# Performance work log

Hardware: AMD Instinct MI355X
Metric: run time of the kernel (lower is better)

Reference implementation:

```python
import jax, jax.numpy as jnp
import numpy as np

B, S, DM = 2, 2048, 1024
H, DH = 16, 64
SCALE = jnp.sqrt(jnp.float32(DH))  # dot_scale = sqrt(dim_head)


def setup_inputs() -> dict:
    key = jax.random.key(0)
    ks = jax.random.split(key, 9)
    std = 1.0 / np.sqrt(DM)
    x = jax.random.normal(ks[0], (B, S, DM), dtype=jnp.float32)
    Wq = jax.random.uniform(ks[1], (DM, DM), jnp.float32, -std, std)
    bq = jax.random.uniform(ks[2], (DM,), jnp.float32, -std, std)
    Wk = jax.random.uniform(ks[3], (DM, DM), jnp.float32, -std, std)
    bk = jax.random.uniform(ks[4], (DM,), jnp.float32, -std, std)
    Wv = jax.random.uniform(ks[5], (DM, DM), jnp.float32, -std, std)
    bv = jax.random.uniform(ks[6], (DM,), jnp.float32, -std, std)
    Wo = jax.random.uniform(ks[7], (DM, DM), jnp.float32, -std, std)
    bo = jax.random.uniform(ks[8], (DM,), jnp.float32, -std, std)
    # causal mask: 1 = masked (future positions), broadcast over batch
    causal = jnp.triu(jnp.ones((S, S), dtype=jnp.int32), k=1)
    attention_mask = jnp.broadcast_to(causal, (B, S, S))
    return {"x": x, "Wq": Wq, "bq": bq, "Wk": Wk, "bk": bk,
            "Wv": Wv, "bv": bv, "Wo": Wo, "bo": bo,
            "attention_mask": attention_mask}


def reference(x, Wq, bq, Wk, bk, Wv, bv, Wo, bo, attention_mask):
    # Linear layers (torch nn.Linear: y = x @ W^T + b)
    q = (x @ Wq.T + bq).reshape(B, S, H, DH).transpose(0, 2, 1, 3)  # (B,H,S,DH)
    k = (x @ Wk.T + bk).reshape(B, S, H, DH).transpose(0, 2, 1, 3)  # (B,H,S,DH)
    v = (x @ Wv.T + bv).reshape(B, S, H, DH).transpose(0, 2, 1, 3)  # (B,H,S,DH)
    # scores: (B,H,S,S), then mask==1 -> -inf, softmax over last dim
    scores = jnp.einsum('bhsd,bhtd->bhst', q, k) / SCALE
    mask = attention_mask[:, None, :, :]  # (B,1,S,S)
    scores = jnp.where(mask == 1, -jnp.inf, scores)
    attn = jax.nn.softmax(scores, axis=-1)
    # dropout is identity in eval mode
    ctx = jnp.einsum('bhst,bhtd->bshd', attn, v).reshape(B, S, H * DH)
    return ctx @ Wo.T + bo
```

## Files before the change

kernel.cpp:

```cpp
#include <hip/hip_runtime.h>
#include <stdint.h>

typedef unsigned short u16;
typedef __attribute__((ext_vector_type(8))) short bf16x8;
typedef __attribute__((ext_vector_type(4))) float f32x4;

#define BATCH 2
#define S_LEN 2048
#define DMODEL 1024
#define NH 16
#define DHEAD 64
#define MTOT 4096
#define QSCALE 0.18033688011112042f
#define PSTR 132

#define GL2LDS(g, l) \
  __builtin_amdgcn_global_load_lds((const __attribute__((address_space(1))) void*)(g), \
                                   (__attribute__((address_space(3))) void*)(l), 16, 0, 0)

__device__ __forceinline__ u16 f2bf(float x) {
  union { float f; uint32_t u; } v; v.f = x;
  uint32_t r = v.u + 0x7fffu + ((v.u >> 16) & 1u);
  return (u16)(r >> 16);
}
__device__ __forceinline__ u16 f2bf_fast(float x) {
  union { float f; uint32_t u; } v; v.f = x;
  return (u16)((v.u + 0x8000u) >> 16);
}

struct CvtArgs {
  const float* src[5];
  u16* dst[5];
};

__global__ __launch_bounds__(256) void cvt_all(CvtArgs a) {
  int bx = blockIdx.x;
  int region, off;
  if (bx < 4096) { region = 0; off = bx; }
  else { region = 1 + ((bx - 4096) >> 10); off = (bx - 4096) & 1023; }
  const float* s = a.src[region];
  u16* d = a.dst[region];
  int i = (off * 256 + threadIdx.x) * 4;
  float4 v = *(const float4*)(s + i);
  uint2 pk;
  pk.x = (uint32_t)f2bf(v.x) | ((uint32_t)f2bf(v.y) << 16);
  pk.y = (uint32_t)f2bf(v.z) | ((uint32_t)f2bf(v.w) << 16);
  *(uint2*)(d + i) = pk;
}

__device__ __forceinline__ void gemm_body(const u16* __restrict__ A,
                                          const u16* __restrict__ W,
                                          const float* __restrict__ bias,
                                          void* __restrict__ out,
                                          int mode, float scale) {
  __shared__ u16 As[128 * 32];
  __shared__ u16 Bs[128 * 32];
  const int tid = threadIdx.x;
  const int m0 = blockIdx.y * 128;
  const int n0 = blockIdx.x * 128;
  const int wave = tid >> 6, lane = tid & 63;
  const int wm = (wave >> 1) * 64, wn = (wave & 1) * 64;
  const int quad = lane >> 4, l15 = lane & 15;

  const int row0 = tid >> 2, k80 = (tid & 3) * 8;
  const int row1 = (tid + 256) >> 2;
  const int lb0 = wave * 512;
  const int lb1 = 2048 + wave * 512;

  f32x4 acc[4][4] = {};

  for (int kt = 0; kt < DMODEL; kt += 32) {
    GL2LDS(A + (size_t)(m0 + row0) * DMODEL + kt + k80, As + lb0);
    GL2LDS(A + (size_t)(m0 + row1) * DMODEL + kt + k80, As + lb1);
    GL2LDS(W + (size_t)(n0 + row0) * DMODEL + kt + k80, Bs + lb0);
    GL2LDS(W + (size_t)(n0 + row1) * DMODEL + kt + k80, Bs + lb1);
    __syncthreads();
    bf16x8 af[4], bfr[4];
#pragma unroll
    for (int bi = 0; bi < 4; ++bi)
      af[bi] = *(const bf16x8*)(&As[(wm + bi * 16 + l15) * 32 + quad * 8]);
#pragma unroll
    for (int bj = 0; bj < 4; ++bj)
      bfr[bj] = *(const bf16x8*)(&Bs[(wn + bj * 16 + l15) * 32 + quad * 8]);
#pragma unroll
    for (int bi = 0; bi < 4; ++bi)
#pragma unroll
      for (int bj = 0; bj < 4; ++bj)
        acc[bi][bj] = __builtin_amdgcn_mfma_f32_16x16x32_bf16(af[bi], bfr[bj], acc[bi][bj], 0, 0, 0);
    __syncthreads();
  }

#pragma unroll
  for (int bi = 0; bi < 4; ++bi) {
#pragma unroll
    for (int bj = 0; bj < 4; ++bj) {
      int n = n0 + wn + bj * 16 + l15;
      float bval = bias[n];
#pragma unroll
      for (int r = 0; r < 4; ++r) {
        int m = m0 + wm + bi * 16 + quad * 4 + r;
        float v = (acc[bi][bj][r] + bval) * scale;
        u16 bvu = f2bf(v);
        int b = m >> 11, s = m & 2047;
        int h = n >> 6, d = n & 63;
        size_t bh = (size_t)(b * NH + h);
        if (mode == 1)
          ((u16*)out)[(bh * S_LEN + s) * DHEAD + d] = bvu;
        else
          ((u16*)out)[((bh * 256 + (s >> 3)) * 64 + d) * 8 + (s & 7)] = bvu;
      }
    }
  }
}

struct QKVArgs {
  const u16* w[3];
  const float* b[3];
  u16* o[3];
};

__global__ __launch_bounds__(256) void qkv_gemm(const u16* __restrict__ xb, QKVArgs a) {
  int z = blockIdx.z;
  int mode = (z == 2) ? 2 : 1;
  float scale = (z == 0) ? QSCALE : 1.0f;
  gemm_body(xb, a.w[z], a.b[z], a.o[z], mode, scale);
}

__global__ __launch_bounds__(256) void out_gemm(const u16* __restrict__ A,
                                                const u16* __restrict__ W,
                                                const float* __restrict__ bias,
                                                float* __restrict__ out) {
  __shared__ u16 As[128 * 32];
  __shared__ u16 Bs[64 * 32];
  const int tid = threadIdx.x;
  const int m0 = blockIdx.y * 128;
  const int n0 = blockIdx.x * 64;
  const int wave = tid >> 6, lane = tid & 63;
  const int wm = (wave >> 1) * 64, wn = (wave & 1) * 32;
  const int quad = lane >> 4, l15 = lane & 15;

  const int row0 = tid >> 2, k80 = (tid & 3) * 8;
  const int row1 = (tid + 256) >> 2;
  const int lb0 = wave * 512;
  const int lb1 = 2048 + wave * 512;

  f32x4 acc[4][2] = {};

  for (int kt = 0; kt < DMODEL; kt += 32) {
    GL2LDS(A + (size_t)(m0 + row0) * DMODEL + kt + k80, As + lb0);
    GL2LDS(A + (size_t)(m0 + row1) * DMODEL + kt + k80, As + lb1);
    GL2LDS(W + (size_t)(n0 + row0) * DMODEL + kt + k80, Bs + lb0);
    __syncthreads();
    bf16x8 af[4], bfr[2];
#pragma unroll
    for (int bi = 0; bi < 4; ++bi)
      af[bi] = *(const bf16x8*)(&As[(wm + bi * 16 + l15) * 32 + quad * 8]);
#pragma unroll
    for (int bj = 0; bj < 2; ++bj)
      bfr[bj] = *(const bf16x8*)(&Bs[(wn + bj * 16 + l15) * 32 + quad * 8]);
#pragma unroll
    for (int bi = 0; bi < 4; ++bi)
#pragma unroll
      for (int bj = 0; bj < 2; ++bj)
        acc[bi][bj] = __builtin_amdgcn_mfma_f32_16x16x32_bf16(af[bi], bfr[bj], acc[bi][bj], 0, 0, 0);
    __syncthreads();
  }

#pragma unroll
  for (int bi = 0; bi < 4; ++bi) {
#pragma unroll
    for (int bj = 0; bj < 2; ++bj) {
      int n = n0 + wn + bj * 16 + l15;
      float bval = bias[n];
#pragma unroll
      for (int r = 0; r < 4; ++r) {
        int m = m0 + wm + bi * 16 + quad * 4 + r;
        out[(size_t)m * DMODEL + n] = acc[bi][bj][r] + bval;
      }
    }
  }
}

__global__ __launch_bounds__(256) void attn(const u16* __restrict__ Q,
                                            const u16* __restrict__ Kg,
                                            const u16* __restrict__ Vt8,
                                            u16* __restrict__ ctx) {
  __shared__ u16 Ks[128 * 72];
  __shared__ u16 Vs[64 * 136];
  __shared__ u16 Ps[64 * PSTR];
  const int tid = threadIdx.x;
  const int qp = blockIdx.x >> 5;
  const int bh = blockIdx.x & 31;
  const int wave = tid >> 6, lane = tid & 63;
  const int quad = lane >> 4, l15 = lane & 15;
  const size_t base = (size_t)bh * S_LEN * DHEAD;
  const int b = bh >> 4, h = bh & 15;

  for (int half = 0; half < 2; ++half) {
    const int qt = half ? (S_LEN / 64 - 1 - qp) : qp;
    const int qrow = qt * 64 + wave * 16 + l15;
    bf16x8 qf0 = *(const bf16x8*)(Q + base + (size_t)qrow * DHEAD + quad * 8);
    bf16x8 qf1 = *(const bf16x8*)(Q + base + (size_t)qrow * DHEAD + 32 + quad * 8);

    float l_part[4] = {0.f, 0.f, 0.f, 0.f};
    f32x4 o[4] = {};

    const int ktmax = qt >> 1;
    for (int kt = 0; kt <= ktmax; ++kt) {
#pragma unroll
      for (int i = 0; i < 4; ++i) {
        int cc = tid + 256 * i;
        {
          int row = cc >> 3, k8 = (cc & 7) * 8;
          uint4 v = *(const uint4*)(Kg + base + (size_t)(kt * 128 + row) * DHEAD + k8);
          *(uint4*)(&Ks[row * 72 + k8]) = v;
        }
        {
          int d = cc & 63, oc = cc >> 6;
          uint4 v = *(const uint4*)(Vt8 + base + (((size_t)(kt * 16 + oc)) * 64 + d) * 8);
          *(uint4*)(&Vs[d * 136 + oc * 8]) = v;
        }
      }
      __syncthreads();

      const bool diag = (kt == ktmax);
      const int qg_max = qt * 64 + wave * 16 + 15;
      f32x4 s_acc[8];
#pragma unroll
      for (int bj = 0; bj < 8; ++bj) {
        if (diag && (kt * 128 + bj * 16 > qg_max)) {
          s_acc[bj] = f32x4{-1e30f, -1e30f, -1e30f, -1e30f};
          continue;
        }
        bf16x8 kf0 = *(const bf16x8*)(&Ks[(bj * 16 + l15) * 72 + quad * 8]);
        bf16x8 kf1 = *(const bf16x8*)(&Ks[(bj * 16 + l15) * 72 + 32 + quad * 8]);
        f32x4 t = {0.f, 0.f, 0.f, 0.f};
        t = __builtin_amdgcn_mfma_f32_16x16x32_bf16(qf0, kf0, t, 0, 0, 0);
        t = __builtin_amdgcn_mfma_f32_16x16x32_bf16(qf1, kf1, t, 0, 0, 0);
        s_acc[bj] = t;
      }

      if (diag) {
#pragma unroll
        for (int bj = 0; bj < 8; ++bj) {
          int kg = kt * 128 + bj * 16 + l15;
#pragma unroll
          for (int r = 0; r < 4; ++r) {
            int qg = qt * 64 + wave * 16 + quad * 4 + r;
            if (kg > qg) s_acc[bj][r] = -1e30f;
          }
        }
      }

#pragma unroll
      for (int bj = 0; bj < 8; ++bj) {
#pragma unroll
        for (int r = 0; r < 4; ++r) {
          float p = exp2f(s_acc[bj][r]);
          l_part[r] += p;
          Ps[(wave * 16 + quad * 4 + r) * PSTR + bj * 16 + l15] = f2bf_fast(p);
        }
      }

#pragma unroll
      for (int kk = 0; kk < 4; ++kk) {
        bf16x8 pf = *(const bf16x8*)(&Ps[(wave * 16 + l15) * PSTR + kk * 32 + quad * 8]);
#pragma unroll
        for (int dj = 0; dj < 4; ++dj) {
          bf16x8 vf = *(const bf16x8*)(&Vs[(dj * 16 + l15) * 136 + kk * 32 + quad * 8]);
          o[dj] = __builtin_amdgcn_mfma_f32_16x16x32_bf16(pf, vf, o[dj], 0, 0, 0);
        }
      }
      __syncthreads();
    }

#pragma unroll
    for (int r = 0; r < 4; ++r) {
      float s = l_part[r];
      s += __shfl_xor(s, 1, 64);
      s += __shfl_xor(s, 2, 64);
      s += __shfl_xor(s, 4, 64);
      s += __shfl_xor(s, 8, 64);
      float inv = 1.0f / s;
      int srow = qt * 64 + wave * 16 + quad * 4 + r;
      size_t rowbase = ((size_t)b * S_LEN + srow) * DMODEL + h * DHEAD;
#pragma unroll
      for (int dj = 0; dj < 4; ++dj)
        ctx[rowbase + dj * 16 + l15] = f2bf(o[dj][r] * inv);
    }
  }
}

extern "C" void kernel_launch(void* const* d_in, const int* in_sizes, int n_in,
                              void* d_out, int out_size, void* d_ws, size_t ws_size,
                              hipStream_t stream) {
  const float* x  = (const float*)d_in[0];
  const float* Wq = (const float*)d_in[1];
  const float* bq = (const float*)d_in[2];
  const float* Wk = (const float*)d_in[3];
  const float* bk = (const float*)d_in[4];
  const float* Wv = (const float*)d_in[5];
  const float* bv = (const float*)d_in[6];
  const float* Wo = (const float*)d_in[7];
  const float* bo = (const float*)d_in[8];
  float* out = (float*)d_out;

  char* ws = (char*)d_ws;
  const size_t MB = 1u << 20;
  u16* xb   = (u16*)(ws + 0);
  u16* ctxb = xb;
  u16* wqb  = (u16*)(ws + 8 * MB);
  u16* wkb  = (u16*)(ws + 10 * MB);
  u16* wvb  = (u16*)(ws + 12 * MB);
  u16* wob  = (u16*)(ws + 14 * MB);
  u16* qb   = (u16*)(ws + 16 * MB);
  u16* kb   = (u16*)(ws + 24 * MB);
  u16* vtb  = (u16*)(ws + 32 * MB);

  CvtArgs c;
  c.src[0] = x;  c.dst[0] = xb;
  c.src[1] = Wq; c.dst[1] = wqb;
  c.src[2] = Wk; c.dst[2] = wkb;
  c.src[3] = Wv; c.dst[3] = wvb;
  c.src[4] = Wo; c.dst[4] = wob;
  cvt_all<<<4096 + 4 * 1024, 256, 0, stream>>>(c);

  QKVArgs a;
  a.w[0] = wqb; a.w[1] = wkb; a.w[2] = wvb;
  a.b[0] = bq;  a.b[1] = bk;  a.b[2] = bv;
  a.o[0] = qb;  a.o[1] = kb;  a.o[2] = vtb;
  qkv_gemm<<<dim3(DMODEL / 128, MTOT / 128, 3), 256, 0, stream>>>(xb, a);

  attn<<<512, 256, 0, stream>>>(qb, kb, vtb, ctxb);

  out_gemm<<<dim3(DMODEL / 64, MTOT / 128), 256, 0, stream>>>(ctxb, wob, bo, out);
}
```

Before: 224.2 us.

## Double GEMM K-tile with XOR-swizzled LDS; split attention to one q-tile per block

Both GEMMs now load 64-wide K tiles per barrier pair, using an XOR swizzle on the LDS column chunk to avoid bank conflicts. This halves the number of sync points per K sweep. The attention kernel drops its paired front/back q-tile loop and launches one block per q-tile, heaviest tiles first. It also aliases the P scratch buffer onto the K tile (with an added barrier) to cut LDS use and raise occupancy. The trade-off is an extra __syncthreads per KV step and a less even per-block workload in attention.

```diff
diff --git a/kernel.cpp b/kernel.cpp
--- a/kernel.cpp
+++ b/kernel.cpp
@@ -53,8 +53,8 @@
                                           const float* __restrict__ bias,
                                           void* __restrict__ out,
                                           int mode, float scale) {
-  __shared__ u16 As[128 * 32];
-  __shared__ u16 Bs[128 * 32];
+  __shared__ u16 As[128 * 64];
+  __shared__ u16 Bs[128 * 64];
   const int tid = threadIdx.x;
   const int m0 = blockIdx.y * 128;
   const int n0 = blockIdx.x * 128;
@@ -62,31 +62,34 @@
   const int wm = (wave >> 1) * 64, wn = (wave & 1) * 64;
   const int quad = lane >> 4, l15 = lane & 15;
 
-  const int row0 = tid >> 2, k80 = (tid & 3) * 8;
-  const int row1 = (tid + 256) >> 2;
-  const int lb0 = wave * 512;
-  const int lb1 = 2048 + wave * 512;
+  const int rr = tid >> 3;
+  const int cl = ((tid & 7) ^ (rr & 7)) * 8;
+  const int xr = (l15 & 7);
 
   f32x4 acc[4][4] = {};
 
-  for (int kt = 0; kt < DMODEL; kt += 32) {
-    GL2LDS(A + (size_t)(m0 + row0) * DMODEL + kt + k80, As + lb0);
-    GL2LDS(A + (size_t)(m0 + row1) * DMODEL + kt + k80, As + lb1);
-    GL2LDS(W + (size_t)(n0 + row0) * DMODEL + kt + k80, Bs + lb0);
-    GL2LDS(W + (size_t)(n0 + row1) * DMODEL + kt + k80, Bs + lb1);
-    __syncthreads();
-    bf16x8 af[4], bfr[4];
-#pragma unroll
-    for (int bi = 0; bi < 4; ++bi)
-      af[bi] = *(const bf16x8*)(&As[(wm + bi * 16 + l15) * 32 + quad * 8]);
-#pragma unroll
-    for (int bj = 0; bj < 4; ++bj)
-      bfr[bj] = *(const bf16x8*)(&Bs[(wn + bj * 16 + l15) * 32 + quad * 8]);
-#pragma unroll
-    for (int bi = 0; bi < 4; ++bi)
+  for (int kt = 0; kt < DMODEL; kt += 64) {
+#pragma unroll
+    for (int j = 0; j < 4; ++j) {
+      GL2LDS(A + (size_t)(m0 + j * 32 + rr) * DMODEL + kt + cl, As + j * 2048 + wave * 512);
+      GL2LDS(W + (size_t)(n0 + j * 32 + rr) * DMODEL + kt + cl, Bs + j * 2048 + wave * 512);
+    }
+    __syncthreads();
+#pragma unroll
+    for (int h = 0; h < 2; ++h) {
+      bf16x8 af[4], bfr[4];
+#pragma unroll
+      for (int bi = 0; bi < 4; ++bi)
+        af[bi] = *(const bf16x8*)(&As[(wm + bi * 16 + l15) * 64 + (((h * 4 + quad) ^ xr) * 8)]);
 #pragma unroll
       for (int bj = 0; bj < 4; ++bj)
-        acc[bi][bj] = __builtin_amdgcn_mfma_f32_16x16x32_bf16(af[bi], bfr[bj], acc[bi][bj], 0, 0, 0);
+        bfr[bj] = *(const bf16x8*)(&Bs[(wn + bj * 16 + l15) * 64 + (((h * 4 + quad) ^ xr) * 8)]);
+#pragma unroll
+      for (int bi = 0; bi < 4; ++bi)
+#pragma unroll
+        for (int bj = 0; bj < 4; ++bj)
+          acc[bi][bj] = __builtin_amdgcn_mfma_f32_16x16x32_bf16(af[bi], bfr[bj], acc[bi][bj], 0, 0, 0);
+    }
     __syncthreads();
   }
 
@@ -130,8 +133,8 @@
                                                 const u16* __restrict__ W,
                                                 const float* __restrict__ bias,
                                                 float* __restrict__ out) {
-  __shared__ u16 As[128 * 32];
-  __shared__ u16 Bs[64 * 32];
+  __shared__ u16 As[128 * 64];
+  __shared__ u16 Bs[64 * 64];
   const int tid = threadIdx.x;
   const int m0 = blockIdx.y * 128;
   const int n0 = blockIdx.x * 64;
@@ -139,30 +142,35 @@
   const int wm = (wave >> 1) * 64, wn = (wave & 1) * 32;
   const int quad = lane >> 4, l15 = lane & 15;
 
-  const int row0 = tid >> 2, k80 = (tid & 3) * 8;
-  const int row1 = (tid + 256) >> 2;
-  const int lb0 = wave * 512;
-  const int lb1 = 2048 + wave * 512;
+  const int rr = tid >> 3;
+  const int cl = ((tid & 7) ^ (rr & 7)) * 8;
+  const int xr = (l15 & 7);
 
   f32x4 acc[4][2] = {};
 
-  for (int kt = 0; kt < DMODEL; kt += 32) {
-    GL2LDS(A + (size_t)(m0 + row0) * DMODEL + kt + k80, As + lb0);
-    GL2LDS(A + (size_t)(m0 + row1) * DMODEL + kt + k80, As + lb1);
-    GL2LDS(W + (size_t)(n0 + row0) * DMODEL + kt + k80, Bs + lb0);
-    __syncthreads();
-    bf16x8 af[4], bfr[2];
-#pragma unroll
-    for (int bi = 0; bi < 4; ++bi)
-      af[bi] = *(const bf16x8*)(&As[(wm + bi * 16 + l15) * 32 + quad * 8]);
-#pragma unroll
-    for (int bj = 0; bj < 2; ++bj)
-      bfr[bj] = *(const bf16x8*)(&Bs[(wn + bj * 16 + l15) * 32 + quad * 8]);
-#pragma unroll
-    for (int bi = 0; bi < 4; ++bi)
+  for (int kt = 0; kt < DMODEL; kt += 64) {
+#pragma unroll
+    for (int j = 0; j < 4; ++j)
+      GL2LDS(A + (size_t)(m0 + j * 32 + rr) * DMODEL + kt + cl, As + j * 2048 + wave * 512);
+#pragma unroll
+    for (int j = 0; j < 2; ++j)
+      GL2LDS(W + (size_t)(n0 + j * 32 + rr) * DMODEL + kt + cl, Bs + j * 2048 + wave * 512);
+    __syncthreads();
+#pragma unroll
+    for (int h = 0; h < 2; ++h) {
+      bf16x8 af[4], bfr[2];
+#pragma unroll
+      for (int bi = 0; bi < 4; ++bi)
+        af[bi] = *(const bf16x8*)(&As[(wm + bi * 16 + l15) * 64 + (((h * 4 + quad) ^ xr) * 8)]);
 #pragma unroll
       for (int bj = 0; bj < 2; ++bj)
-        acc[bi][bj] = __builtin_amdgcn_mfma_f32_16x16x32_bf16(af[bi], bfr[bj], acc[bi][bj], 0, 0, 0);
+        bfr[bj] = *(const bf16x8*)(&Bs[(wn + bj * 16 + l15) * 64 + (((h * 4 + quad) ^ xr) * 8)]);
+#pragma unroll
+      for (int bi = 0; bi < 4; ++bi)
+#pragma unroll
+        for (int bj = 0; bj < 2; ++bj)
+          acc[bi][bj] = __builtin_amdgcn_mfma_f32_16x16x32_bf16(af[bi], bfr[bj], acc[bi][bj], 0, 0, 0);
+    }
     __syncthreads();
   }
 
@@ -187,73 +195,78 @@
                                             u16* __restrict__ ctx) {
   __shared__ u16 Ks[128 * 72];
   __shared__ u16 Vs[64 * 136];
-  __shared__ u16 Ps[64 * PSTR];
+  u16* Ps = Ks;
   const int tid = threadIdx.x;
-  const int qp = blockIdx.x >> 5;
+  const int qt = 31 - (blockIdx.x >> 5);
   const int bh = blockIdx.x & 31;
   const int wave = tid >> 6, lane = tid & 63;
   const int quad = lane >> 4, l15 = lane & 15;
   const size_t base = (size_t)bh * S_LEN * DHEAD;
   const int b = bh >> 4, h = bh & 15;
 
-  for (int half = 0; half < 2; ++half) {
-    const int qt = half ? (S_LEN / 64 - 1 - qp) : qp;
-    const int qrow = qt * 64 + wave * 16 + l15;
-    bf16x8 qf0 = *(const bf16x8*)(Q + base + (size_t)qrow * DHEAD + quad * 8);
-    bf16x8 qf1 = *(const bf16x8*)(Q + base + (size_t)qrow * DHEAD + 32 + quad * 8);
-
-    float l_part[4] = {0.f, 0.f, 0.f, 0.f};
-    f32x4 o[4] = {};
-
-    const int ktmax = qt >> 1;
-    for (int kt = 0; kt <= ktmax; ++kt) {
-#pragma unroll
-      for (int i = 0; i < 4; ++i) {
-        int cc = tid + 256 * i;
-        {
-          int row = cc >> 3, k8 = (cc & 7) * 8;
-          uint4 v = *(const uint4*)(Kg + base + (size_t)(kt * 128 + row) * DHEAD + k8);
-          *(uint4*)(&Ks[row * 72 + k8]) = v;
+  const int qrow = qt * 64 + wave * 16 + l15;
+  bf16x8 qf0 = *(const bf16x8*)(Q + base + (size_t)qrow * DHEAD + quad * 8);
+  bf16x8 qf1 = *(const bf16x8*)(Q + base + (size_t)qrow * DHEAD + 32 + quad * 8);
+
+  float l_part[4] = {0.f, 0.f, 0.f, 0.f};
+  f32x4 o[4] = {};
+
+  const int ktmax = qt >> 1;
+  for (int kt = 0; kt <= ktmax; ++kt) {
+#pragma unroll
+    for (int i = 0; i < 4; ++i) {
+      int cc = tid + 256 * i;
+      {
+        int row = cc >> 3, k8 = (cc & 7) * 8;
+        uint4 v = *(const uint4*)(Kg + base + (size_t)(kt * 128 + row) * DHEAD + k8);
+        *(uint4*)(&Ks[row * 72 + k8]) = v;
+      }
+      {
+        int d = cc & 63, oc = cc >> 6;
+        uint4 v = *(const uint4*)(Vt8 + base + (((size_t)(kt * 16 + oc)) * 64 + d) * 8);
+        *(uint4*)(&Vs[d * 136 + oc * 8]) = v;
+      }
+    }
+    __syncthreads();
+
+    const bool diag = (kt == ktmax);
+    const int qg_max = qt * 64 + wave * 16 + 15;
+    f32x4 s_acc[8];
+#pragma unroll
+    for (int bj = 0; bj < 8; ++bj) {
+      if (diag && (kt * 128 + bj * 16 > qg_max)) {
+        s_acc[bj] = f32x4{-1e30f, -1e30f, -1e30f, -1e30f};
+        continue;
+      }
+      bf16x8 kf0 = *(const bf16x8*)(&Ks[(bj * 16 + l15) * 72 + quad * 8]);
+      bf16x8 kf1 = *(const bf16x8*)(&Ks[(bj * 16 + l15) * 72 + 32 + quad * 8]);
+      f32x4 t = {0.f, 0.f, 0.f, 0.f};
+      t = __builtin_amdgcn_mfma_f32_16x16x32_bf16(qf0, kf0, t, 0, 0, 0);
+      t = __builtin_amdgcn_mfma_f32_16x16x32_bf16(qf1, kf1, t, 0, 0, 0);
+      s_acc[bj] = t;
+    }
+
+    if (diag) {
+#pragma unroll
+      for (int bj = 0; bj < 8; ++bj) {
+        int kg = kt * 128 + bj * 16 + l15;
+#pragma unroll
+        for (int r = 0; r < 4; ++r) {
+          int qg = qt * 64 + wave * 16 + quad * 4 + r;
+          if (kg > qg) s_acc[bj][r] = -1e30f;
         }
-        {
-          int d = cc & 63, oc = cc >> 6;
-          uint4 v = *(const uint4*)(Vt8 + base + (((size_t)(kt * 16 + oc)) * 64 + d) * 8);
-          *(uint4*)(&Vs[d * 136 + oc * 8]) = v;
-        }
-      }
-      __syncthreads();
-
-      const bool diag = (kt == ktmax);
-      const int qg_max = qt * 64 + wave * 16 + 15;
-      f32x4 s_acc[8];
-#pragma unroll
-      for (int bj = 0; bj < 8; ++bj) {
-        if (diag && (kt * 128 + bj * 16 > qg_max)) {
-          s_acc[bj] = f32x4{-1e30f, -1e30f, -1e30f, -1e30f};
-          continue;
-        }
-        bf16x8 kf0 = *(const bf16x8*)(&Ks[(bj * 16 + l15) * 72 + quad * 8]);
-        bf16x8 kf1 = *(const bf16x8*)(&Ks[(bj * 16 + l15) * 72 + 32 + quad * 8]);
-        f32x4 t = {0.f, 0.f, 0.f, 0.f};
-        t = __builtin_amdgcn_mfma_f32_16x16x32_bf16(qf0, kf0, t, 0, 0, 0);
-        t = __builtin_amdgcn_mfma_f32_16x16x32_bf16(qf1, kf1, t, 0, 0, 0);
-        s_acc[bj] = t;
-      }
-
-      if (diag) {
-#pragma unroll
-        for (int bj = 0; bj < 8; ++bj) {
-          int kg = kt * 128 + bj * 16 + l15;
-#pragma unroll
-          for (int r = 0; r < 4; ++r) {
-            int qg = qt * 64 + wave * 16 + quad * 4 + r;
-            if (kg > qg) s_acc[bj][r] = -1e30f;
-          }
-        }
-      }
-
-#pragma unroll
-      for (int bj = 0; bj < 8; ++bj) {
+      }
+    }
+
+    __syncthreads();
+
+#pragma unroll
+    for (int bj = 0; bj < 8; ++bj) {
+      if (diag && (kt * 128 + bj * 16 > qg_max)) {
+#pragma unroll
+        for (int r = 0; r < 4; ++r)
+          Ps[(wave * 16 + quad * 4 + r) * PSTR + bj * 16 + l15] = 0;
+      } else {
 #pragma unroll
         for (int r = 0; r < 4; ++r) {
           float p = exp2f(s_acc[bj][r]);
@@ -261,33 +274,33 @@
           Ps[(wave * 16 + quad * 4 + r) * PSTR + bj * 16 + l15] = f2bf_fast(p);
         }
       }
-
-#pragma unroll
-      for (int kk = 0; kk < 4; ++kk) {
-        bf16x8 pf = *(const bf16x8*)(&Ps[(wave * 16 + l15) * PSTR + kk * 32 + quad * 8]);
-#pragma unroll
-        for (int dj = 0; dj < 4; ++dj) {
-          bf16x8 vf = *(const bf16x8*)(&Vs[(dj * 16 + l15) * 136 + kk * 32 + quad * 8]);
-          o[dj] = __builtin_amdgcn_mfma_f32_16x16x32_bf16(pf, vf, o[dj], 0, 0, 0);
-        }
-      }
-      __syncthreads();
-    }
-
-#pragma unroll
-    for (int r = 0; r < 4; ++r) {
-      float s = l_part[r];
-      s += __shfl_xor(s, 1, 64);
-      s += __shfl_xor(s, 2, 64);
-      s += __shfl_xor(s, 4, 64);
-      s += __shfl_xor(s, 8, 64);
-      float inv = 1.0f / s;
-      int srow = qt * 64 + wave * 16 + quad * 4 + r;
-      size_t rowbase = ((size_t)b * S_LEN + srow) * DMODEL + h * DHEAD;
-#pragma unroll
-      for (int dj = 0; dj < 4; ++dj)
-        ctx[rowbase + dj * 16 + l15] = f2bf(o[dj][r] * inv);
-    }
+    }
+
+#pragma unroll
+    for (int kk = 0; kk < 4; ++kk) {
+      bf16x8 pf = *(const bf16x8*)(&Ps[(wave * 16 + l15) * PSTR + kk * 32 + quad * 8]);
+#pragma unroll
+      for (int dj = 0; dj < 4; ++dj) {
+        bf16x8 vf = *(const bf16x8*)(&Vs[(dj * 16 + l15) * 136 + kk * 32 + quad * 8]);
+        o[dj] = __builtin_amdgcn_mfma_f32_16x16x32_bf16(pf, vf, o[dj], 0, 0, 0);
+      }
+    }
+    __syncthreads();
+  }
+
+#pragma unroll
+  for (int r = 0; r < 4; ++r) {
+    float s = l_part[r];
+    s += __shfl_xor(s, 1, 64);
+    s += __shfl_xor(s, 2, 64);
+    s += __shfl_xor(s, 4, 64);
+    s += __shfl_xor(s, 8, 64);
+    float inv = 1.0f / s;
+    int srow = qt * 64 + wave * 16 + quad * 4 + r;
+    size_t rowbase = ((size_t)b * S_LEN + srow) * DMODEL + h * DHEAD;
+#pragma unroll
+    for (int dj = 0; dj < 4; ++dj)
+      ctx[rowbase + dj * 16 + l15] = f2bf(o[dj][r] * inv);
   }
 }
 
@@ -331,7 +344,7 @@
   a.o[0] = qb;  a.o[1] = kb;  a.o[2] = vtb;
   qkv_gemm<<<dim3(DMODEL / 128, MTOT / 128, 3), 256, 0, stream>>>(xb, a);
 
-  attn<<<512, 256, 0, stream>>>(qb, kb, vtb, ctxb);
+  attn<<<1024, 256, 0, stream>>>(qb, kb, vtb, ctxb);
 
   out_gemm<<<dim3(DMODEL / 64, MTOT / 128), 256, 0, stream>>>(ctxb, wob, bo, out);
 }
```

After: 243.7 us. 8.7% more time.

## Double-buffer attention K/V via direct-to-LDS loads and XOR-swizzle GEMM LDS tiles

Applied to the files above, without the earlier changes.

The attention kernel now stages K and V tiles with global_load_lds into double-buffered LDS, prefetching the next tile while the current one is computed. It drops the per-tile trailing barrier. K rows use an XOR swizzle to avoid bank conflicts, and V is read in its native 8-packed layout. The PV step is split into two 64-key halves so fully masked halves on the diagonal tile skip their exp and MFMA work. Both GEMMs also XOR-swizzle their LDS tile columns to reduce bank conflicts on fragment reads. The cost is more LDS use, which may lower occupancy, plus the sync correctness of the single-barrier pipeline and the reuse of the P buffer.

```diff
diff --git a/kernel.cpp b/kernel.cpp
--- a/kernel.cpp
+++ b/kernel.cpp
@@ -12,7 +12,6 @@
 #define DHEAD 64
 #define MTOT 4096
 #define QSCALE 0.18033688011112042f
-#define PSTR 132
 
 #define GL2LDS(g, l) \
   __builtin_amdgcn_global_load_lds((const __attribute__((address_space(1))) void*)(g), \
@@ -62,26 +61,27 @@
   const int wm = (wave >> 1) * 64, wn = (wave & 1) * 64;
   const int quad = lane >> 4, l15 = lane & 15;
 
-  const int row0 = tid >> 2, k80 = (tid & 3) * 8;
-  const int row1 = (tid + 256) >> 2;
+  const int row0 = tid >> 2, g0 = ((tid & 3) ^ (row0 & 3)) * 8;
+  const int row1 = (tid + 256) >> 2, g1 = ((tid & 3) ^ (row1 & 3)) * 8;
   const int lb0 = wave * 512;
   const int lb1 = 2048 + wave * 512;
+  const int xk = (quad ^ (l15 & 3)) * 8;
 
   f32x4 acc[4][4] = {};
 
   for (int kt = 0; kt < DMODEL; kt += 32) {
-    GL2LDS(A + (size_t)(m0 + row0) * DMODEL + kt + k80, As + lb0);
-    GL2LDS(A + (size_t)(m0 + row1) * DMODEL + kt + k80, As + lb1);
-    GL2LDS(W + (size_t)(n0 + row0) * DMODEL + kt + k80, Bs + lb0);
-    GL2LDS(W + (size_t)(n0 + row1) * DMODEL + kt + k80, Bs + lb1);
+    GL2LDS(A + (size_t)(m0 + row0) * DMODEL + kt + g0, As + lb0);
+    GL2LDS(A + (size_t)(m0 + row1) * DMODEL + kt + g1, As + lb1);
+    GL2LDS(W + (size_t)(n0 + row0) * DMODEL + kt + g0, Bs + lb0);
+    GL2LDS(W + (size_t)(n0 + row1) * DMODEL + kt + g1, Bs + lb1);
     __syncthreads();
     bf16x8 af[4], bfr[4];
 #pragma unroll
     for (int bi = 0; bi < 4; ++bi)
-      af[bi] = *(const bf16x8*)(&As[(wm + bi * 16 + l15) * 32 + quad * 8]);
+      af[bi] = *(const bf16x8*)(&As[(wm + bi * 16 + l15) * 32 + xk]);
 #pragma unroll
     for (int bj = 0; bj < 4; ++bj)
-      bfr[bj] = *(const bf16x8*)(&Bs[(wn + bj * 16 + l15) * 32 + quad * 8]);
+      bfr[bj] = *(const bf16x8*)(&Bs[(wn + bj * 16 + l15) * 32 + xk]);
 #pragma unroll
     for (int bi = 0; bi < 4; ++bi)
 #pragma unroll
@@ -139,25 +139,26 @@
   const int wm = (wave >> 1) * 64, wn = (wave & 1) * 32;
   const int quad = lane >> 4, l15 = lane & 15;
 
-  const int row0 = tid >> 2, k80 = (tid & 3) * 8;
-  const int row1 = (tid + 256) >> 2;
+  const int row0 = tid >> 2, g0 = ((tid & 3) ^ (row0 & 3)) * 8;
+  const int row1 = (tid + 256) >> 2, g1 = ((tid & 3) ^ (row1 & 3)) * 8;
   const int lb0 = wave * 512;
   const int lb1 = 2048 + wave * 512;
+  const int xk = (quad ^ (l15 & 3)) * 8;
 
   f32x4 acc[4][2] = {};
 
   for (int kt = 0; kt < DMODEL; kt += 32) {
-    GL2LDS(A + (size_t)(m0 + row0) * DMODEL + kt + k80, As + lb0);
-    GL2LDS(A + (size_t)(m0 + row1) * DMODEL + kt + k80, As + lb1);
-    GL2LDS(W + (size_t)(n0 + row0) * DMODEL + kt + k80, Bs + lb0);
+    GL2LDS(A + (size_t)(m0 + row0) * DMODEL + kt + g0, As + lb0);
+    GL2LDS(A + (size_t)(m0 + row1) * DMODEL + kt + g1, As + lb1);
+    GL2LDS(W + (size_t)(n0 + row0) * DMODEL + kt + g0, Bs + lb0);
     __syncthreads();
     bf16x8 af[4], bfr[2];
 #pragma unroll
     for (int bi = 0; bi < 4; ++bi)
-      af[bi] = *(const bf16x8*)(&As[(wm + bi * 16 + l15) * 32 + quad * 8]);
+      af[bi] = *(const bf16x8*)(&As[(wm + bi * 16 + l15) * 32 + xk]);
 #pragma unroll
     for (int bj = 0; bj < 2; ++bj)
-      bfr[bj] = *(const bf16x8*)(&Bs[(wn + bj * 16 + l15) * 32 + quad * 8]);
+      bfr[bj] = *(const bf16x8*)(&Bs[(wn + bj * 16 + l15) * 32 + xk]);
 #pragma unroll
     for (int bi = 0; bi < 4; ++bi)
 #pragma unroll
@@ -185,9 +186,9 @@
                                             const u16* __restrict__ Kg,
                                             const u16* __restrict__ Vt8,
                                             u16* __restrict__ ctx) {
-  __shared__ u16 Ks[128 * 72];
-  __shared__ u16 Vs[64 * 136];
-  __shared__ u16 Ps[64 * PSTR];
+  __shared__ u16 Kd[2][128 * 64];
+  __shared__ u16 Vd[2][64 * 128];
+  __shared__ u16 Ps[64 * 80];
   const int tid = threadIdx.x;
   const int qp = blockIdx.x >> 5;
   const int bh = blockIdx.x & 31;
@@ -195,9 +196,23 @@
   const int quad = lane >> 4, l15 = lane & 15;
   const size_t base = (size_t)bh * S_LEN * DHEAD;
   const int b = bh >> 4, h = bh & 15;
+  const int xk7 = l15 & 7;
+
+#define STAGE(kt_, pb)                                                                   \
+  do {                                                                                   \
+    _Pragma("unroll")                                                                    \
+    for (int i_ = 0; i_ < 4; ++i_) {                                                     \
+      int c_ = tid + 256 * i_;                                                           \
+      int row_ = c_ >> 3, g_ = ((c_ & 7) ^ (row_ & 7)) * 8;                              \
+      GL2LDS(Kg + base + (size_t)((kt_) * 128 + row_) * 64 + g_,                         \
+             &Kd[pb][0] + i_ * 2048 + wave * 512);                                       \
+      GL2LDS(Vt8 + base + (size_t)((kt_) * 1024 + c_) * 8,                               \
+             &Vd[pb][0] + i_ * 2048 + wave * 512);                                       \
+    }                                                                                    \
+  } while (0)
 
   for (int half = 0; half < 2; ++half) {
-    const int qt = half ? (S_LEN / 64 - 1 - qp) : qp;
+    const int qt = half ? (31 - qp) : qp;
     const int qrow = qt * 64 + wave * 16 + l15;
     bf16x8 qf0 = *(const bf16x8*)(Q + base + (size_t)qrow * DHEAD + quad * 8);
     bf16x8 qf1 = *(const bf16x8*)(Q + base + (size_t)qrow * DHEAD + 32 + quad * 8);
@@ -206,22 +221,12 @@
     f32x4 o[4] = {};
 
     const int ktmax = qt >> 1;
+    STAGE(0, 0);
+
     for (int kt = 0; kt <= ktmax; ++kt) {
-#pragma unroll
-      for (int i = 0; i < 4; ++i) {
-        int cc = tid + 256 * i;
-        {
-          int row = cc >> 3, k8 = (cc & 7) * 8;
-          uint4 v = *(const uint4*)(Kg + base + (size_t)(kt * 128 + row) * DHEAD + k8);
-          *(uint4*)(&Ks[row * 72 + k8]) = v;
-        }
-        {
-          int d = cc & 63, oc = cc >> 6;
-          uint4 v = *(const uint4*)(Vt8 + base + (((size_t)(kt * 16 + oc)) * 64 + d) * 8);
-          *(uint4*)(&Vs[d * 136 + oc * 8]) = v;
-        }
-      }
+      const int p = kt & 1;
       __syncthreads();
+      if (kt < ktmax) STAGE(kt + 1, p ^ 1);
 
       const bool diag = (kt == ktmax);
       const int qg_max = qt * 64 + wave * 16 + 15;
@@ -232,8 +237,9 @@
           s_acc[bj] = f32x4{-1e30f, -1e30f, -1e30f, -1e30f};
           continue;
         }
-        bf16x8 kf0 = *(const bf16x8*)(&Ks[(bj * 16 + l15) * 72 + quad * 8]);
-        bf16x8 kf1 = *(const bf16x8*)(&Ks[(bj * 16 + l15) * 72 + 32 + quad * 8]);
+        const int krow = (bj * 16 + l15) * 64;
+        bf16x8 kf0 = *(const bf16x8*)(&Kd[p][krow + ((quad ^ xk7) * 8)]);
+        bf16x8 kf1 = *(const bf16x8*)(&Kd[p][krow + (((quad + 4) ^ xk7) * 8)]);
         f32x4 t = {0.f, 0.f, 0.f, 0.f};
         t = __builtin_amdgcn_mfma_f32_16x16x32_bf16(qf0, kf0, t, 0, 0, 0);
         t = __builtin_amdgcn_mfma_f32_16x16x32_bf16(qf1, kf1, t, 0, 0, 0);
@@ -253,26 +259,32 @@
       }
 
 #pragma unroll
-      for (int bj = 0; bj < 8; ++bj) {
-#pragma unroll
-        for (int r = 0; r < 4; ++r) {
-          float p = exp2f(s_acc[bj][r]);
-          l_part[r] += p;
-          Ps[(wave * 16 + quad * 4 + r) * PSTR + bj * 16 + l15] = f2bf_fast(p);
+      for (int ph = 0; ph < 2; ++ph) {
+        if (diag && (kt * 128 + ph * 64 > qg_max)) continue;
+#pragma unroll
+        for (int bj2 = 0; bj2 < 4; ++bj2) {
+          int bj = ph * 4 + bj2;
+#pragma unroll
+          for (int r = 0; r < 4; ++r) {
+            float pv = exp2f(s_acc[bj][r]);
+            l_part[r] += pv;
+            Ps[(wave * 16 + quad * 4 + r) * 80 + bj2 * 16 + l15] = f2bf_fast(pv);
+          }
         }
-      }
-
-#pragma unroll
-      for (int kk = 0; kk < 4; ++kk) {
-        bf16x8 pf = *(const bf16x8*)(&Ps[(wave * 16 + l15) * PSTR + kk * 32 + quad * 8]);
-#pragma unroll
-        for (int dj = 0; dj < 4; ++dj) {
-          bf16x8 vf = *(const bf16x8*)(&Vs[(dj * 16 + l15) * 136 + kk * 32 + quad * 8]);
-          o[dj] = __builtin_amdgcn_mfma_f32_16x16x32_bf16(pf, vf, o[dj], 0, 0, 0);
+#pragma unroll
+        for (int kk2 = 0; kk2 < 2; ++kk2) {
+          bf16x8 pf = *(const bf16x8*)(&Ps[(wave * 16 + l15) * 80 + kk2 * 32 + quad * 8]);
+          int kk = ph * 2 + kk2;
+#pragma unroll
+          for (int dj = 0; dj < 4; ++dj) {
+            bf16x8 vf = *(const bf16x8*)(&Vd[p][((kk * 4 + quad) * 64 + dj * 16 + l15) * 8]);
+            o[dj] = __builtin_amdgcn_mfma_f32_16x16x32_bf16(pf, vf, o[dj], 0, 0, 0);
+          }
         }
       }
-      __syncthreads();
     }
+
+    __syncthreads();
 
 #pragma unroll
     for (int r = 0; r < 4; ++r) {
@@ -289,6 +301,7 @@
         ctx[rowbase + dj * 16 + l15] = f2bf(o[dj][r] * inv);
     }
   }
+#undef STAGE
 }
 
 extern "C" void kernel_launch(void* const* d_in, const int* in_sizes, int n_in,
```

Result: faster. 209.2 us (-6.7%).
